# Optimization experiments

Measured on AMD Instinct MI355X. Metric: run time of the kernel, lower is better.

## Reference

```python
import jax, jax.numpy as jnp
import numpy as np

T, B, F, H = 256, 128, 1024, 1024  # time (orig dim0), batch (orig dim1), input, hidden


def _xavier(key, shape):
    fan_in, fan_out = shape
    limit = float(np.sqrt(6.0 / (fan_in + fan_out)))
    return jax.random.uniform(key, shape, jnp.float32, -limit, limit)


def setup_inputs() -> dict:
    key = jax.random.key(0)
    k1, k2, k3 = jax.random.split(key, 3)
    return {
        "x": jax.random.normal(k1, (T, B, F), dtype=jnp.float32),
        "h0": jnp.zeros((H,), jnp.float32),
        "c0": jnp.zeros((H,), jnp.float32),
        "weight_ih": _xavier(k2, (F, 4 * H)),
        "weight_hh": _xavier(k3, (H, 4 * H)),
        "bias": jnp.zeros((4 * H,), jnp.float32),
    }


def reference(x, h0, c0, weight_ih, weight_hh, bias):
    # Faithful to the torch code: due to its transpose+index quirk, the
    # recurrence runs over the ORIGINAL dim 0 (time=T) with dim 1 as batch.
    hs = H
    h_init = jnp.broadcast_to(h0, (B, hs))
    c_init = jnp.broadcast_to(c0, (B, hs))

    def step(carry, x_t):  # x_t: (B, F)
        h, c = carry
        gates = x_t @ weight_ih + h @ weight_hh + bias  # (B, 4H)
        i = jax.nn.sigmoid(gates[:, :hs])
        f = jax.nn.sigmoid(gates[:, hs:2 * hs])
        g = jnp.tanh(gates[:, 2 * hs:3 * hs])
        o = jax.nn.sigmoid(gates[:, 3 * hs:])
        c_new = f * c + i * g
        h_new = o * jnp.tanh(c_new)
        return (h_new, c_new), h_new

    (h_t, c_t), hidden_seq = jax.lax.scan(step, (h_init, c_init), x)
    return hidden_seq, h_t, c_t  # hidden_seq: (T, B, H)
```

## Files before the change

kernel.cpp:

```cpp
#include <hip/hip_runtime.h>
#include <hip/hip_bf16.h>


typedef __attribute__((ext_vector_type(8))) short short8;
typedef __attribute__((ext_vector_type(4))) float floatx4;

#define HID_OFF 33554432L
#define CT_OFF  33685504L
#define WTAIL_F 29360128L

__device__ __forceinline__ unsigned short f2bf(float f) {
    __hip_bfloat16 hb = __float2bfloat16(f);
    return *reinterpret_cast<unsigned short*>(&hb);
}

__device__ __forceinline__ uint4 pack8(const float* p) {
    float4 f0 = *reinterpret_cast<const float4*>(p);
    float4 f1 = *reinterpret_cast<const float4*>(p + 4);
    union { uint4 v; unsigned short u[8]; } t;
    t.u[0] = f2bf(f0.x); t.u[1] = f2bf(f0.y); t.u[2] = f2bf(f0.z); t.u[3] = f2bf(f0.w);
    t.u[4] = f2bf(f1.x); t.u[5] = f2bf(f1.y); t.u[6] = f2bf(f1.z); t.u[7] = f2bf(f1.w);
    return t.v;
}

__global__ void pack_w_kernel(const float* __restrict__ wih,
                              const float* __restrict__ whh,
                              unsigned short* __restrict__ pB) {
    int g    = blockIdx.x * 256 + threadIdx.x;
    int lane = g & 63;
    int frag = g >> 6;
    int kblk = frag & 63;
    int nblk = frag >> 6;
    int n = nblk * 16 + (lane & 15);
    int k = kblk * 32 + ((lane >> 4) << 3);
    const float* src = (k < 1024) ? (wih + (size_t)k * 4096 + n)
                                  : (whh + (size_t)(k - 1024) * 4096 + n);
    __attribute__((aligned(16))) unsigned short tmp[8];
#pragma unroll
    for (int jj = 0; jj < 8; ++jj) tmp[jj] = f2bf(src[(size_t)jj * 4096]);
    *reinterpret_cast<uint4*>(pB + (size_t)frag * 512 + lane * 8) =
        *reinterpret_cast<const uint4*>(tmp);
}

__global__ void pack_x_kernel(const float* __restrict__ x,
                              unsigned short* __restrict__ pX) {
    int g    = blockIdx.x * 256 + threadIdx.x;
    int lane = g & 63;
    int frag = g >> 6;
    int kblk = frag & 31;
    int mblk = (frag >> 5) & 7;
    int t    = frag >> 8;
    int m = mblk * 16 + (lane & 15);
    int k = kblk * 32 + ((lane >> 4) << 3);
    *reinterpret_cast<uint4*>(pX + (size_t)frag * 512 + lane * 8) =
        pack8(x + (size_t)(t * 128 + m) * 1024 + k);
}

__global__ void pack_h0_kernel(const float* __restrict__ h0,
                               unsigned short* __restrict__ pH) {
    int g    = blockIdx.x * 256 + threadIdx.x;
    int lane = g & 63;
    int frag = g >> 6;
    int kblk = frag & 31;
    int k = kblk * 32 + ((lane >> 4) << 3);
    __attribute__((aligned(16))) unsigned short tmp[8];
#pragma unroll
    for (int jj = 0; jj < 8; ++jj) tmp[jj] = f2bf(h0[k + jj]);
    *reinterpret_cast<uint4*>(pH + (size_t)frag * 512 + lane * 8) =
        *reinterpret_cast<const uint4*>(tmp);
}

__global__ __launch_bounds__(256, 1) void lstm_main(
    const float* __restrict__ x, const float* __restrict__ h0,
    const float* __restrict__ c0, const float* __restrict__ bias,
    const unsigned short* __restrict__ pB,
    unsigned short* pH, int use_ph,
    const unsigned short* __restrict__ pX, int use_px,
    float* out, int* cnt) {

    __shared__ __align__(16) unsigned short Abuf[2][32][512];
    __shared__ float g_lds[4][32][17];
    __shared__ float c_lds[32][16];
    __shared__ __align__(16) unsigned short hbf_lds[32][16];

    const int tid  = threadIdx.x;
    const int lane = tid & 63;
    const int w    = tid >> 6;
    const int wg   = blockIdx.x;
    const int r    = (wg >> 3) & 3;
    const int j    = (wg & 7) * 8 + (wg >> 5);
    const int col  = lane & 15;
    const int quad = lane >> 4;
    const int nblk = w * 64 + j;

    int* subp = cnt + (r * 8 + (j >> 3)) * 64;
    int* relp = cnt + (32 + r) * 64;
    const bool is_agg = (j == 0);

    const float breg = bias[w * 1024 + j * 16 + col];

    {
        float cv = c0[j * 16 + (tid & 15)];
        int row = tid >> 4;
        c_lds[row][tid & 15]      = cv;
        c_lds[row + 16][tid & 15] = cv;
    }

    const unsigned short* pBw = pB + (size_t)nblk * 64 * 512 + lane * 8;
    short8 bw[64];
#pragma unroll
    for (int kb = 0; kb < 64; ++kb)
        bw[kb] = *reinterpret_cast<const short8*>(pBw + (size_t)kb * 512);

    auto stage_x_full = [&](int tt) {
#pragma unroll
        for (int i = 0; i < 16; ++i) {
            int s = tid + 256 * i;
            int ln = s & 63, kbg = (s >> 6) & 31, mb = s >> 11;
            if (use_px) {
                const unsigned short* src =
                    pX + (((size_t)(tt * 8 + 2 * r + mb) * 32 + kbg) * 512) + ln * 8;
                *reinterpret_cast<uint4*>(&Abuf[mb][kbg][ln * 8]) =
                    *reinterpret_cast<const uint4*>(src);
            } else {
                int m = 32 * r + mb * 16 + (ln & 15);
                int k = kbg * 32 + ((ln >> 4) << 3);
                *reinterpret_cast<uint4*>(&Abuf[mb][kbg][ln * 8]) =
                    pack8(x + (size_t)(tt * 128 + m) * 1024 + k);
            }
        }
    };

    auto stage_h_full = [&](int tt) {
        if (use_ph) {
            const unsigned long long* hb = reinterpret_cast<const unsigned long long*>(
                pH + (size_t)(tt & 1) * 131072);
#pragma unroll
            for (int c = 0; c < 2; ++c) {
                unsigned long long v[16];
#pragma unroll
                for (int i = 0; i < 8; ++i) {
                    int s = tid + 256 * (c * 8 + i);
                    int ln = s & 63, kbg = (s >> 6) & 31, mb = s >> 11;
                    size_t u = (((size_t)(2 * r + mb) * 32 + kbg) * 512 + ln * 8) >> 2;
                    v[2 * i]     = __hip_atomic_load(hb + u, __ATOMIC_RELAXED,
                                                     __HIP_MEMORY_SCOPE_AGENT);
                    v[2 * i + 1] = __hip_atomic_load(hb + u + 1, __ATOMIC_RELAXED,
                                                     __HIP_MEMORY_SCOPE_AGENT);
                }
#pragma unroll
                for (int i = 0; i < 8; ++i) {
                    int s = tid + 256 * (c * 8 + i);
                    int ln = s & 63, kbg = (s >> 6) & 31, mb = s >> 11;
                    unsigned long long* dp =
                        reinterpret_cast<unsigned long long*>(&Abuf[mb][kbg][ln * 8]);
                    dp[0] = v[2 * i];
                    dp[1] = v[2 * i + 1];
                }
            }
        } else {
#pragma unroll
            for (int i = 0; i < 16; ++i) {
                int s = tid + 256 * i;
                int ln = s & 63, kbg = (s >> 6) & 31, mb = s >> 11;
                if (tt == 0) {
                    int k = kbg * 32 + ((ln >> 4) << 3);
                    union { uint4 v; unsigned short u[8]; } tv;
#pragma unroll
                    for (int jj = 0; jj < 8; ++jj) tv.u[jj] = f2bf(h0[k + jj]);
                    *reinterpret_cast<uint4*>(&Abuf[mb][kbg][ln * 8]) = tv.v;
                } else {
                    int m = 32 * r + mb * 16 + (ln & 15);
                    int k = kbg * 32 + ((ln >> 4) << 3);
                    *reinterpret_cast<uint4*>(&Abuf[mb][kbg][ln * 8]) =
                        pack8(out + (size_t)(tt - 1) * 131072 + (size_t)m * 1024 + k);
                }
            }
        }
    };

    auto gemm_x = [&](floatx4& A0, floatx4& A1) {
#pragma unroll
        for (int kb = 0; kb < 32; ++kb) {
            short8 a0 = *reinterpret_cast<const short8*>(&Abuf[0][kb][lane * 8]);
            short8 a1 = *reinterpret_cast<const short8*>(&Abuf[1][kb][lane * 8]);
            A0 = __builtin_amdgcn_mfma_f32_16x16x32_bf16(a0, bw[kb], A0, 0, 0, 0);
            A1 = __builtin_amdgcn_mfma_f32_16x16x32_bf16(a1, bw[kb], A1, 0, 0, 0);
        }
    };
    auto gemm_h = [&](floatx4& A0, floatx4& A1) {
#pragma unroll
        for (int kb = 0; kb < 32; ++kb) {
            short8 a0 = *reinterpret_cast<const short8*>(&Abuf[0][kb][lane * 8]);
            short8 a1 = *reinterpret_cast<const short8*>(&Abuf[1][kb][lane * 8]);
            A0 = __builtin_amdgcn_mfma_f32_16x16x32_bf16(a0, bw[32 + kb], A0, 0, 0, 0);
            A1 = __builtin_amdgcn_mfma_f32_16x16x32_bf16(a1, bw[32 + kb], A1, 0, 0, 0);
        }
    };

    floatx4 xa0 = {0.f, 0.f, 0.f, 0.f}, xa1 = {0.f, 0.f, 0.f, 0.f};

    __syncthreads();
    stage_x_full(0);
    __syncthreads();
    gemm_x(xa0, xa1);

    for (int t = 0; t < 256; ++t) {
        floatx4 acc0 = xa0, acc1 = xa1;

        if (t > 0 && tid == 0) {
            while (__hip_atomic_load(relp, __ATOMIC_RELAXED,
                                     __HIP_MEMORY_SCOPE_AGENT) < t)
                __builtin_amdgcn_s_sleep(1);
            if (!use_ph)
                __builtin_amdgcn_fence(__ATOMIC_ACQUIRE, "agent");
        }
        __syncthreads();

        stage_h_full(t);
        __syncthreads();
        gemm_h(acc0, acc1);

#pragma unroll
        for (int rr = 0; rr < 4; ++rr) {
            float p0 = acc0[rr] + breg;
            float p1 = acc1[rr] + breg;
            float v0, v1;
            if (w == 2) { v0 = tanhf(p0); v1 = tanhf(p1); }
            else        { v0 = 1.f / (1.f + __expf(-p0)); v1 = 1.f / (1.f + __expf(-p1)); }
            g_lds[w][quad * 4 + rr][col]      = v0;
            g_lds[w][16 + quad * 4 + rr][col] = v1;
        }
        __syncthreads();

        {
            const long hidbase = (long)t * 131072;
#pragma unroll
            for (int p = 0; p < 2; ++p) {
                int row = p * 16 + (tid >> 4);
                int cc  = tid & 15;
                float iv = g_lds[0][row][cc];
                float fv = g_lds[1][row][cc];
                float gv = g_lds[2][row][cc];
                float ov = g_lds[3][row][cc];
                float cold = c_lds[row][cc];
                float cnew = fv * cold + iv * gv;
                float hv   = ov * tanhf(cnew);
                c_lds[row][cc]   = cnew;
                hbf_lds[row][cc] = f2bf(hv);
                int m = 32 * r + row;
                out[hidbase + (long)m * 1024 + j * 16 + cc] = hv;
                if (t == 255) {
                    out[HID_OFF + (long)m * 1024 + j * 16 + cc] = hv;
                    out[CT_OFF  + (long)m * 1024 + j * 16 + cc] = cnew;
                }
            }
        }
        __syncthreads();

        if (t < 255) {
            if (use_ph && tid < 64) {
                int ml = tid >> 1, cg = tid & 1;
                int m = 32 * r + ml, kcol = j * 16 + cg * 8;
                int frag  = (2 * r + (ml >> 4)) * 32 + (kcol >> 5);
                int lanep = (m & 15) + 16 * ((kcol & 31) >> 3);
                unsigned short* dst = pH + (size_t)((t & 1) ^ 1) * 131072 +
                                      (size_t)frag * 512 + lanep * 8;
                const unsigned long long* sv =
                    reinterpret_cast<const unsigned long long*>(&hbf_lds[ml][cg * 8]);
                unsigned long long* d64 = reinterpret_cast<unsigned long long*>(dst);
                __hip_atomic_store(d64, sv[0], __ATOMIC_RELAXED,
                                   __HIP_MEMORY_SCOPE_AGENT);
                __hip_atomic_store(d64 + 1, sv[1], __ATOMIC_RELAXED,
                                   __HIP_MEMORY_SCOPE_AGENT);
            }
            if (tid == 0) {
                if (use_ph) {
                    asm volatile("s_waitcnt vmcnt(0)" ::: "memory");
                    __hip_atomic_fetch_add(subp, 1, __ATOMIC_RELAXED,
                                           __HIP_MEMORY_SCOPE_AGENT);
                } else {
                    __hip_atomic_fetch_add(subp, 1, __ATOMIC_RELEASE,
                                           __HIP_MEMORY_SCOPE_AGENT);
                }
            }

            xa0 = (floatx4){0.f, 0.f, 0.f, 0.f};
            xa1 = (floatx4){0.f, 0.f, 0.f, 0.f};
            stage_x_full(t + 1);
            __syncthreads();
            gemm_x(xa0, xa1);

            if (is_agg && tid < 8) {
                int* sp = cnt + (r * 8 + tid) * 64;
                int target = 8 * (t + 1);
                while (true) {
                    int v = __hip_atomic_load(sp, __ATOMIC_RELAXED,
                                              __HIP_MEMORY_SCOPE_AGENT);
                    if (__ballot(v >= target) == 0xFFull) break;
                    __builtin_amdgcn_s_sleep(1);
                }
                if (!use_ph)
                    __builtin_amdgcn_fence(__ATOMIC_ACQUIRE, "agent");
                asm volatile("" ::: "memory");
                if (tid == 0) {
                    if (use_ph)
                        __hip_atomic_store(relp, t + 1, __ATOMIC_RELAXED,
                                           __HIP_MEMORY_SCOPE_AGENT);
                    else
                        __hip_atomic_store(relp, t + 1, __ATOMIC_RELEASE,
                                           __HIP_MEMORY_SCOPE_AGENT);
                }
            }
        }
    }
}

extern "C" void kernel_launch(void* const* d_in, const int* in_sizes, int n_in,
                              void* d_out, int out_size, void* d_ws, size_t ws_size,
                              hipStream_t stream) {
    (void)in_sizes; (void)n_in; (void)out_size;
    const float* x    = (const float*)d_in[0];
    const float* h0   = (const float*)d_in[1];
    const float* c0   = (const float*)d_in[2];
    const float* wih  = (const float*)d_in[3];
    const float* whh  = (const float*)d_in[4];
    const float* bias = (const float*)d_in[5];
    float* out = (float*)d_out;

    char* ws = (char*)d_ws;
    int* counters = (int*)ws;
    const size_t SZB = 2048ull * 4096 * 2;
    const size_t SZH = 2ull * 256 * 512 * 2;
    const size_t SZX = 65536ull * 512 * 2;

    size_t off = 16384;
    unsigned short* pB;
    if (ws_size >= off + SZB) {
        pB = (unsigned short*)(ws + off); off += SZB;
    } else {
        pB = (unsigned short*)(out + WTAIL_F);
    }
    int use_ph = (ws_size >= off + SZH) ? 1 : 0;
    unsigned short* pH = use_ph ? (unsigned short*)(ws + off) : (unsigned short*)0;
    if (use_ph) off += SZH;
    int use_px = (ws_size >= off + SZX) ? 1 : 0;
    unsigned short* pX = use_px ? (unsigned short*)(ws + off) : (unsigned short*)0;

    hipMemsetAsync(ws, 0, 16384, stream);
    pack_w_kernel<<<4096, 256, 0, stream>>>(wih, whh, pB);
    if (use_ph) pack_h0_kernel<<<64, 256, 0, stream>>>(h0, pH);
    if (use_px) pack_x_kernel<<<16384, 256, 0, stream>>>(x, pX);

    lstm_main<<<dim3(256), dim3(256), 0, stream>>>(
        x, h0, c0, bias, pB, pH, use_ph, pX, use_px, out, counters);
}
```

Measured before the change: 3.324 ms.

## Replace aggregator-based step barrier with direct per-block counter polling

Removes the two-level barrier, where one aggregator block per row group waited on sub-counters and then published a release flag. Every block now polls the eight sub-counters itself with a ballot. The fp32 hidden-state store to the output is moved after the bf16 handoff write when the packed path is active, so the critical handoff is published earlier. The h0 pack kernel is dropped, and step 0 converts h0 directly. The h staging loads are merged into one batch of 32 in-flight loads. The trade-off is more polling traffic on the shared counters and higher register pressure.

```diff
diff --git a/kernel.cpp b/kernel.cpp
--- a/kernel.cpp
+++ b/kernel.cpp
@@ -56,20 +56,6 @@
         pack8(x + (size_t)(t * 128 + m) * 1024 + k);
 }
 
-__global__ void pack_h0_kernel(const float* __restrict__ h0,
-                               unsigned short* __restrict__ pH) {
-    int g    = blockIdx.x * 256 + threadIdx.x;
-    int lane = g & 63;
-    int frag = g >> 6;
-    int kblk = frag & 31;
-    int k = kblk * 32 + ((lane >> 4) << 3);
-    __attribute__((aligned(16))) unsigned short tmp[8];
-#pragma unroll
-    for (int jj = 0; jj < 8; ++jj) tmp[jj] = f2bf(h0[k + jj]);
-    *reinterpret_cast<uint4*>(pH + (size_t)frag * 512 + lane * 8) =
-        *reinterpret_cast<const uint4*>(tmp);
-}
-
 __global__ __launch_bounds__(256, 1) void lstm_main(
     const float* __restrict__ x, const float* __restrict__ h0,
     const float* __restrict__ c0, const float* __restrict__ bias,
@@ -94,8 +80,6 @@
     const int nblk = w * 64 + j;
 
     int* subp = cnt + (r * 8 + (j >> 3)) * 64;
-    int* relp = cnt + (32 + r) * 64;
-    const bool is_agg = (j == 0);
 
     const float breg = bias[w * 1024 + j * 16 + col];
 
@@ -132,49 +116,49 @@
     };
 
     auto stage_h_full = [&](int tt) {
-        if (use_ph) {
-            const unsigned long long* hb = reinterpret_cast<const unsigned long long*>(
-                pH + (size_t)(tt & 1) * 131072);
-#pragma unroll
-            for (int c = 0; c < 2; ++c) {
-                unsigned long long v[16];
-#pragma unroll
-                for (int i = 0; i < 8; ++i) {
-                    int s = tid + 256 * (c * 8 + i);
-                    int ln = s & 63, kbg = (s >> 6) & 31, mb = s >> 11;
-                    size_t u = (((size_t)(2 * r + mb) * 32 + kbg) * 512 + ln * 8) >> 2;
-                    v[2 * i]     = __hip_atomic_load(hb + u, __ATOMIC_RELAXED,
-                                                     __HIP_MEMORY_SCOPE_AGENT);
-                    v[2 * i + 1] = __hip_atomic_load(hb + u + 1, __ATOMIC_RELAXED,
-                                                     __HIP_MEMORY_SCOPE_AGENT);
-                }
-#pragma unroll
-                for (int i = 0; i < 8; ++i) {
-                    int s = tid + 256 * (c * 8 + i);
-                    int ln = s & 63, kbg = (s >> 6) & 31, mb = s >> 11;
-                    unsigned long long* dp =
-                        reinterpret_cast<unsigned long long*>(&Abuf[mb][kbg][ln * 8]);
-                    dp[0] = v[2 * i];
-                    dp[1] = v[2 * i + 1];
-                }
-            }
-        } else {
+        if (tt == 0) {
 #pragma unroll
             for (int i = 0; i < 16; ++i) {
                 int s = tid + 256 * i;
                 int ln = s & 63, kbg = (s >> 6) & 31, mb = s >> 11;
-                if (tt == 0) {
-                    int k = kbg * 32 + ((ln >> 4) << 3);
-                    union { uint4 v; unsigned short u[8]; } tv;
-#pragma unroll
-                    for (int jj = 0; jj < 8; ++jj) tv.u[jj] = f2bf(h0[k + jj]);
-                    *reinterpret_cast<uint4*>(&Abuf[mb][kbg][ln * 8]) = tv.v;
-                } else {
-                    int m = 32 * r + mb * 16 + (ln & 15);
-                    int k = kbg * 32 + ((ln >> 4) << 3);
-                    *reinterpret_cast<uint4*>(&Abuf[mb][kbg][ln * 8]) =
-                        pack8(out + (size_t)(tt - 1) * 131072 + (size_t)m * 1024 + k);
-                }
+                int k = kbg * 32 + ((ln >> 4) << 3);
+                union { uint4 v; unsigned short u[8]; } tv;
+#pragma unroll
+                for (int jj = 0; jj < 8; ++jj) tv.u[jj] = f2bf(h0[k + jj]);
+                *reinterpret_cast<uint4*>(&Abuf[mb][kbg][ln * 8]) = tv.v;
+            }
+        } else if (use_ph) {
+            const unsigned long long* hb = reinterpret_cast<const unsigned long long*>(
+                pH + (size_t)(tt & 1) * 131072);
+            unsigned long long v[32];
+#pragma unroll
+            for (int i = 0; i < 16; ++i) {
+                int s = tid + 256 * i;
+                int ln = s & 63, kbg = (s >> 6) & 31, mb = s >> 11;
+                size_t u = (((size_t)(2 * r + mb) * 32 + kbg) * 512 + ln * 8) >> 2;
+                v[2 * i]     = __hip_atomic_load(hb + u, __ATOMIC_RELAXED,
+                                                 __HIP_MEMORY_SCOPE_AGENT);
+                v[2 * i + 1] = __hip_atomic_load(hb + u + 1, __ATOMIC_RELAXED,
+                                                 __HIP_MEMORY_SCOPE_AGENT);
+            }
+#pragma unroll
+            for (int i = 0; i < 16; ++i) {
+                int s = tid + 256 * i;
+                int ln = s & 63, kbg = (s >> 6) & 31, mb = s >> 11;
+                unsigned long long* dp =
+                    reinterpret_cast<unsigned long long*>(&Abuf[mb][kbg][ln * 8]);
+                dp[0] = v[2 * i];
+                dp[1] = v[2 * i + 1];
+            }
+        } else {
+#pragma unroll
+            for (int i = 0; i < 16; ++i) {
+                int s = tid + 256 * i;
+                int ln = s & 63, kbg = (s >> 6) & 31, mb = s >> 11;
+                int m = 32 * r + mb * 16 + (ln & 15);
+                int k = kbg * 32 + ((ln >> 4) << 3);
+                *reinterpret_cast<uint4*>(&Abuf[mb][kbg][ln * 8]) =
+                    pack8(out + (size_t)(tt - 1) * 131072 + (size_t)m * 1024 + k);
             }
         }
     };
@@ -208,10 +192,15 @@
     for (int t = 0; t < 256; ++t) {
         floatx4 acc0 = xa0, acc1 = xa1;
 
-        if (t > 0 && tid == 0) {
-            while (__hip_atomic_load(relp, __ATOMIC_RELAXED,
-                                     __HIP_MEMORY_SCOPE_AGENT) < t)
+        if (t > 0 && tid < 8) {
+            int* sp = cnt + (r * 8 + tid) * 64;
+            const int target = 8 * t;
+            while (true) {
+                int vv = __hip_atomic_load(sp, __ATOMIC_RELAXED,
+                                           __HIP_MEMORY_SCOPE_AGENT);
+                if (__ballot(vv >= target) == 0xFFull) break;
                 __builtin_amdgcn_s_sleep(1);
+            }
             if (!use_ph)
                 __builtin_amdgcn_fence(__ATOMIC_ACQUIRE, "agent");
         }
@@ -233,30 +222,43 @@
         }
         __syncthreads();
 
+        const int row0 = tid >> 4, cc = tid & 15;
+        float hv0, hv1, cn0, cn1;
         {
+            float iv = g_lds[0][row0][cc];
+            float fv = g_lds[1][row0][cc];
+            float gv = g_lds[2][row0][cc];
+            float ov = g_lds[3][row0][cc];
+            cn0 = fv * c_lds[row0][cc] + iv * gv;
+            hv0 = ov * tanhf(cn0);
+            c_lds[row0][cc]   = cn0;
+            hbf_lds[row0][cc] = f2bf(hv0);
+            int row1 = row0 + 16;
+            iv = g_lds[0][row1][cc];
+            fv = g_lds[1][row1][cc];
+            gv = g_lds[2][row1][cc];
+            ov = g_lds[3][row1][cc];
+            cn1 = fv * c_lds[row1][cc] + iv * gv;
+            hv1 = ov * tanhf(cn1);
+            c_lds[row1][cc]   = cn1;
+            hbf_lds[row1][cc] = f2bf(hv1);
+        }
+        __syncthreads();
+
+        auto store_out = [&]() {
             const long hidbase = (long)t * 131072;
-#pragma unroll
-            for (int p = 0; p < 2; ++p) {
-                int row = p * 16 + (tid >> 4);
-                int cc  = tid & 15;
-                float iv = g_lds[0][row][cc];
-                float fv = g_lds[1][row][cc];
-                float gv = g_lds[2][row][cc];
-                float ov = g_lds[3][row][cc];
-                float cold = c_lds[row][cc];
-                float cnew = fv * cold + iv * gv;
-                float hv   = ov * tanhf(cnew);
-                c_lds[row][cc]   = cnew;
-                hbf_lds[row][cc] = f2bf(hv);
-                int m = 32 * r + row;
-                out[hidbase + (long)m * 1024 + j * 16 + cc] = hv;
-                if (t == 255) {
-                    out[HID_OFF + (long)m * 1024 + j * 16 + cc] = hv;
-                    out[CT_OFF  + (long)m * 1024 + j * 16 + cc] = cnew;
-                }
-            }
-        }
-        __syncthreads();
+            const long m0 = 32 * r + row0, m1 = m0 + 16;
+            out[hidbase + m0 * 1024 + j * 16 + cc] = hv0;
+            out[hidbase + m1 * 1024 + j * 16 + cc] = hv1;
+            if (t == 255) {
+                out[HID_OFF + m0 * 1024 + j * 16 + cc] = hv0;
+                out[HID_OFF + m1 * 1024 + j * 16 + cc] = hv1;
+                out[CT_OFF  + m0 * 1024 + j * 16 + cc] = cn0;
+                out[CT_OFF  + m1 * 1024 + j * 16 + cc] = cn1;
+            }
+        };
+
+        if (!use_ph) store_out();
 
         if (t < 255) {
             if (use_ph && tid < 64) {
@@ -284,34 +286,16 @@
                                            __HIP_MEMORY_SCOPE_AGENT);
                 }
             }
-
+        }
+
+        if (use_ph) store_out();
+
+        if (t < 255) {
             xa0 = (floatx4){0.f, 0.f, 0.f, 0.f};
             xa1 = (floatx4){0.f, 0.f, 0.f, 0.f};
             stage_x_full(t + 1);
             __syncthreads();
             gemm_x(xa0, xa1);
-
-            if (is_agg && tid < 8) {
-                int* sp = cnt + (r * 8 + tid) * 64;
-                int target = 8 * (t + 1);
-                while (true) {
-                    int v = __hip_atomic_load(sp, __ATOMIC_RELAXED,
-                                              __HIP_MEMORY_SCOPE_AGENT);
-                    if (__ballot(v >= target) == 0xFFull) break;
-                    __builtin_amdgcn_s_sleep(1);
-                }
-                if (!use_ph)
-                    __builtin_amdgcn_fence(__ATOMIC_ACQUIRE, "agent");
-                asm volatile("" ::: "memory");
-                if (tid == 0) {
-                    if (use_ph)
-                        __hip_atomic_store(relp, t + 1, __ATOMIC_RELAXED,
-                                           __HIP_MEMORY_SCOPE_AGENT);
-                    else
-                        __hip_atomic_store(relp, t + 1, __ATOMIC_RELEASE,
-                                           __HIP_MEMORY_SCOPE_AGENT);
-                }
-            }
         }
     }
 }
@@ -349,7 +333,6 @@
 
     hipMemsetAsync(ws, 0, 16384, stream);
     pack_w_kernel<<<4096, 256, 0, stream>>>(wih, whh, pB);
-    if (use_ph) pack_h0_kernel<<<64, 256, 0, stream>>>(h0, pH);
     if (use_px) pack_x_kernel<<<16384, 256, 0, stream>>>(x, pX);
 
     lstm_main<<<dim3(256), dim3(256), 0, stream>>>(
```

Measured after the change: 3.231 ms. 1.03x faster.
